# Kernel optimization log

Measured on AMD Instinct MI355X. Metric: run time of the kernel, lower is better.

## Reference

```python
import jax, jax.numpy as jnp
import numpy as np
import math

EMBED_DIM = 1024
N_HEADS = 16
HEAD_DIM = EMBED_DIM // N_HEADS
B, N = 2, 2048


def setup_inputs() -> dict:
    key = jax.random.key(0)
    k1, k2, k3 = jax.random.split(key, 3)
    x = jax.random.normal(k1, (B, N, EMBED_DIM), dtype=jnp.float32)
    # Per-head Linear(D, 3*head_dim), stacked over heads. PyTorch Linear init scale ~1/sqrt(fan_in).
    bound = 1.0 / math.sqrt(EMBED_DIM)
    Wkqv = jax.random.uniform(k2, (N_HEADS, EMBED_DIM, 3 * HEAD_DIM), dtype=jnp.float32, minval=-bound, maxval=bound)
    bkqv = jax.random.uniform(k3, (N_HEADS, 3 * HEAD_DIM), dtype=jnp.float32, minval=-bound, maxval=bound)
    return {"x": x, "Wkqv": Wkqv, "bkqv": bkqv}


def reference(x, Wkqv, bkqv):
    Bx, Nx, D = x.shape
    hd = Wkqv.shape[-1] // 3
    # all heads at once: [B, H, N, 3*hd]
    proj = jnp.einsum('bnd,hdf->bhnf', x, Wkqv) + bkqv[None, :, None, :]
    # torch.split order in the original is (k, q, v)
    k, q, v = jnp.split(proj, 3, axis=-1)
    # scores = q @ k^T / sqrt(head_dim)   [B, H, N, N]
    scores = jnp.einsum('bhqd,bhkd->bhqk', q, k) / math.sqrt(hd)
    causal = jnp.tril(jnp.ones((Nx, Nx), dtype=bool))
    scores = jnp.where(causal[None, None, :, :], scores, -jnp.inf)
    attn = jax.nn.softmax(scores, axis=-1)
    out = jnp.einsum('bhqk,bhkd->bhqd', attn, v)  # [B, H, N, hd]
    # concat heads -> [B, N, D]  (forward() passes no out_matrix, so no output projection)
    return out.transpose(0, 2, 1, 3).reshape(Bx, Nx, D)
```

## Files before the change

### kernel.cpp

```cpp
#include <hip/hip_runtime.h>
#include <math.h>

typedef float f32x4 __attribute__((ext_vector_type(4)));
typedef __bf16 bf16x8 __attribute__((ext_vector_type(8)));
typedef __bf16 bf16x4 __attribute__((ext_vector_type(4)));

#define MFMA16(a, b, c) __builtin_amdgcn_mfma_f32_16x16x32_bf16((a), (b), (c), 0, 0, 0)

constexpr int Bsz = 2, Nseq = 2048, Dm = 1024, Hh = 16, HDim = 64, F3 = 192;
constexpr int Mrows = Bsz * Nseq;
constexpr int NC = Hh * F3;
constexpr float QSCALE = 0.125f * 1.4426950408889634f;

__device__ inline void load_lds16(const void* g, void* l) {
    __builtin_amdgcn_global_load_lds((const __attribute__((address_space(1))) void*)g,
                                     (__attribute__((address_space(3))) void*)l, 16, 0, 0);
}

#define FENCE asm volatile("" ::: "memory")
#define BARRIER do { FENCE; __builtin_amdgcn_s_barrier(); FENCE; } while (0)


__global__ __launch_bounds__(256) void conv_xw_kernel(const float* __restrict__ x,
                                                      __bf16* __restrict__ xb,
                                                      const float* __restrict__ w,
                                                      __bf16* __restrict__ wt) {
    __shared__ __bf16 tile[32][66];
    if (blockIdx.x < 2048) {
        int i = blockIdx.x * 256 + threadIdx.x;
        const float4* xv = reinterpret_cast<const float4*>(x);
        float4 a = xv[2 * i];
        float4 b = xv[2 * i + 1];
        bf16x8 o = {(__bf16)a.x, (__bf16)a.y, (__bf16)a.z, (__bf16)a.w,
                    (__bf16)b.x, (__bf16)b.y, (__bf16)b.z, (__bf16)b.w};
        *reinterpret_cast<bf16x8*>(xb + 8 * i) = o;
    } else {
        int id = blockIdx.x - 2048;
        int h = id / 96, rem = id % 96;
        int d0 = (rem & 31) * 32, c0 = (rem >> 5) * 64;
        for (int i = threadIdx.x; i < 32 * 64; i += 256) {
            int di = i >> 6, cj = i & 63;
            tile[di][cj] = (__bf16)w[(size_t)(h * Dm + d0 + di) * F3 + c0 + cj];
        }
        __syncthreads();
        for (int i = threadIdx.x; i < 32 * 64; i += 256) {
            int ci = i >> 5, dj = i & 31;
            wt[(size_t)(h * F3 + c0 + ci) * Dm + d0 + dj] = tile[dj][ci];
        }
    }
}

__global__ __launch_bounds__(256) void conv_w_kernel(const float* __restrict__ w,
                                                     __bf16* __restrict__ wt) {
    __shared__ __bf16 tile[32][66];
    int h = blockIdx.z, d0 = blockIdx.x * 32, c0 = blockIdx.y * 64;
    for (int i = threadIdx.x; i < 32 * 64; i += 256) {
        int di = i >> 6, cj = i & 63;
        tile[di][cj] = (__bf16)w[(size_t)(h * Dm + d0 + di) * F3 + c0 + cj];
    }
    __syncthreads();
    for (int i = threadIdx.x; i < 32 * 64; i += 256) {
        int ci = i >> 5, dj = i & 31;
        wt[(size_t)(h * F3 + c0 + ci) * Dm + d0 + dj] = tile[dj][ci];
    }
}

__global__ __launch_bounds__(512, 4) void gemm_proj(const __bf16* __restrict__ xb,
                                                    const __bf16* __restrict__ wt,
                                                    const float* __restrict__ bias,
                                                    __bf16* __restrict__ kbuf,
                                                    __bf16* __restrict__ qbuf,
                                                    __bf16* __restrict__ vt) {
    __shared__ __align__(16) __bf16 Ab[2][128 * 64];
    __shared__ __align__(16) __bf16 Bb[2][192 * 64];

    int flat = blockIdx.x;
    int swz = (flat & 7) * 64 + (flat >> 3);
    int bm = swz >> 4, bn = swz & 15;
    int r0 = bm * 128, n0 = bn * 192;

    int w = threadIdx.x >> 6, lane = threadIdx.x & 63;
    int col = lane & 15, quad = lane >> 4;
    int wm = w >> 2, wn = w & 3;

    f32x4 acc[4][3] = {};

    int rl = lane >> 3;
    int cg = ((lane & 7) ^ rl) * 8;

    auto stage = [&](int t, int s) {
#pragma unroll
        for (int i = 0; i < 2; i++) {
            int rowb = w * 16 + i * 8;
            load_lds16(xb + (size_t)(r0 + rowb + rl) * Dm + t * 64 + cg,
                       &Ab[s][rowb * 64]);
        }
#pragma unroll
        for (int i = 0; i < 3; i++) {
            int rowb = w * 24 + i * 8;
            load_lds16(wt + (size_t)(n0 + rowb + rl) * Dm + t * 64 + cg,
                       &Bb[s][rowb * 64]);
        }
    };

    stage(0, 0);
    stage(1, 1);

    for (int j = 0; j < 16; j++) {
        int s = j & 1;
        if (j < 15) asm volatile("s_waitcnt vmcnt(5)" ::: "memory");
        else        asm volatile("s_waitcnt vmcnt(0)" ::: "memory");
        BARRIER;

#pragma unroll
        for (int ks = 0; ks < 2; ks++) {
            int cq = ks * 4 + quad;
            bf16x8 af[4], bfr[3];
#pragma unroll
            for (int mt = 0; mt < 4; mt++) {
                int row = wm * 64 + mt * 16 + col;
                af[mt] = *reinterpret_cast<const bf16x8*>(
                    &Ab[s][row * 64 + ((cq ^ (row & 7)) * 8)]);
            }
#pragma unroll
            for (int nt = 0; nt < 3; nt++) {
                int row = wn * 48 + nt * 16 + col;
                bfr[nt] = *reinterpret_cast<const bf16x8*>(
                    &Bb[s][row * 64 + ((cq ^ (row & 7)) * 8)]);
            }
            __builtin_amdgcn_s_setprio(1);
#pragma unroll
            for (int mt = 0; mt < 4; mt++)
#pragma unroll
                for (int nt = 0; nt < 3; nt++)
                    acc[mt][nt] = MFMA16(af[mt], bfr[nt], acc[mt][nt]);
            __builtin_amdgcn_s_setprio(0);
        }

        BARRIER;
        if (j + 2 < 16) stage(j + 2, s);
    }

#pragma unroll
    for (int nt = 0; nt < 3; nt++) {
        int g = n0 + wn * 48 + nt * 16 + col;
        int h = g / F3, c = g - h * F3;
        float bv = bias[g];
        bool isq = (c >= 64 && c < 128), isv = (c >= 128);
        int cd = c & 63;
#pragma unroll
        for (int mt = 0; mt < 4; mt++) {
#pragma unroll
            for (int rg = 0; rg < 4; rg++) {
                int r = r0 + wm * 64 + mt * 16 + quad * 4 + rg;
                int b = r >> 11, n = r & (Nseq - 1);
                float v = acc[mt][nt][rg] + bv;
                if (isq) v *= QSCALE;
                size_t bh = (size_t)(b * Hh + h);
                if (isv) {
                    int np = (n & ~63) | ((n & 15) << 2) | ((n >> 4) & 3);
                    vt[(bh * HDim + cd) * Nseq + np] = (__bf16)v;
                } else {
                    ((isq) ? qbuf : kbuf)[(bh * Nseq + n) * HDim + cd] = (__bf16)v;
                }
            }
        }
    }
}

__global__ __launch_bounds__(256) void proj_small(const float* __restrict__ x,
                                                  const __bf16* __restrict__ wt,
                                                  const float* __restrict__ bias,
                                                  __bf16* __restrict__ kbuf,
                                                  __bf16* __restrict__ qbuf,
                                                  __bf16* __restrict__ vt) {
    int h = blockIdx.y;
    int wave = threadIdx.x >> 6, lane = threadIdx.x & 63;
    int col = lane & 15, quad = lane >> 4;
    int r0 = blockIdx.x * 128 + wave * 32;

    f32x4 acc[12][2] = {};
    const float* xr0 = x + (size_t)(r0 + col) * Dm + quad * 8;
    const float* xr1 = xr0 + 16 * Dm;
    const __bf16* wbase = wt + (size_t)(h * F3 + col) * Dm + quad * 8;

    for (int k0 = 0; k0 < Dm; k0 += 32) {
        float4 a0lo = *reinterpret_cast<const float4*>(xr0 + k0);
        float4 a0hi = *reinterpret_cast<const float4*>(xr0 + k0 + 4);
        float4 a1lo = *reinterpret_cast<const float4*>(xr1 + k0);
        float4 a1hi = *reinterpret_cast<const float4*>(xr1 + k0 + 4);
        bf16x8 a0 = {(__bf16)a0lo.x, (__bf16)a0lo.y, (__bf16)a0lo.z, (__bf16)a0lo.w,
                     (__bf16)a0hi.x, (__bf16)a0hi.y, (__bf16)a0hi.z, (__bf16)a0hi.w};
        bf16x8 a1 = {(__bf16)a1lo.x, (__bf16)a1lo.y, (__bf16)a1lo.z, (__bf16)a1lo.w,
                     (__bf16)a1hi.x, (__bf16)a1hi.y, (__bf16)a1hi.z, (__bf16)a1hi.w};
#pragma unroll
        for (int ct = 0; ct < 12; ct++) {
            bf16x8 bf = *reinterpret_cast<const bf16x8*>(wbase + ct * 16 * Dm + k0);
            acc[ct][0] = MFMA16(a0, bf, acc[ct][0]);
            acc[ct][1] = MFMA16(a1, bf, acc[ct][1]);
        }
    }
#pragma unroll
    for (int ct = 0; ct < 12; ct++) {
        int c = ct * 16 + col;
        float bv = bias[h * F3 + c];
        int cd = c & 63;
        bool isq = (c >= 64 && c < 128), isv = (c >= 128);
#pragma unroll
        for (int rt = 0; rt < 2; rt++) {
#pragma unroll
            for (int rg = 0; rg < 4; rg++) {
                int r = r0 + rt * 16 + quad * 4 + rg;
                int b = r >> 11, n = r & (Nseq - 1);
                float v = acc[ct][rt][rg] + bv;
                if (isq) v *= QSCALE;
                size_t bh = (size_t)(b * Hh + h);
                if (isv) {
                    int np = (n & ~63) | ((n & 15) << 2) | ((n >> 4) & 3);
                    vt[(bh * HDim + cd) * Nseq + np] = (__bf16)v;
                } else {
                    ((isq) ? qbuf : kbuf)[(bh * Nseq + n) * HDim + cd] = (__bf16)v;
                }
            }
        }
    }
}

__global__ __launch_bounds__(256) void attn_kernel(const __bf16* __restrict__ qbuf,
                                                   const __bf16* __restrict__ kbuf,
                                                   const __bf16* __restrict__ vt,
                                                   float* __restrict__ out) {
    __shared__ __align__(16) __bf16 Kb[2][64 * 64];
    __shared__ __align__(16) __bf16 Vb[2][64 * 64];
    __shared__ __align__(16) __bf16 plds[4][16 * 64];
    int bh = blockIdx.x;
    int b = bh >> 4, h = bh & 15;
    int tile = 31 - blockIdx.y;
    int wave = threadIdx.x >> 6, lane = threadIdx.x & 63;
    int col = lane & 15, quad = lane >> 4;
    int q0 = tile * 64 + wave * 16;

    const __bf16* qbase = qbuf + (size_t)bh * Nseq * HDim;
    const __bf16* kbase = kbuf + (size_t)bh * Nseq * HDim;
    const __bf16* vbase = vt + (size_t)bh * HDim * Nseq;

    bf16x8 aq0 = *reinterpret_cast<const bf16x8*>(qbase + (q0 + col) * HDim + quad * 8);
    bf16x8 aq1 = *reinterpret_cast<const bf16x8*>(qbase + (q0 + col) * HDim + quad * 8 + 32);

    const bf16x8 vone = {(__bf16)1.f, (__bf16)1.f, (__bf16)1.f, (__bf16)1.f,
                         (__bf16)1.f, (__bf16)1.f, (__bf16)1.f, (__bf16)1.f};

    f32x4 o[4] = {};
    f32x4 ls = {};

    int mb = tile * 64;
    int loop_end = mb + 64;

    int rl = lane >> 3;
    int srow0 = wave * 16 + rl;
    int srow1 = wave * 16 + 8 + rl;
    int sc = (lane & 7) ^ rl;
    const __bf16* ksrc0 = kbase + srow0 * HDim + sc * 8;
    const __bf16* ksrc1 = kbase + srow1 * HDim + sc * 8;
    const __bf16* vsrc0 = vbase + (size_t)srow0 * Nseq + sc * 8;
    const __bf16* vsrc1 = vbase + (size_t)srow1 * Nseq + sc * 8;
    int d0 = wave * 1024, d1 = wave * 1024 + 512;

    int sw0 = ((quad ^ (col & 7)) * 8);
    int sw1 = (((quad + 4) ^ (col & 7)) * 8);

    int pr0 = col * 64 + ((quad ^ (col & 7)) << 3);
    int pr1 = col * 64 + (((quad + 4) ^ (col & 7)) << 3);

    load_lds16(ksrc0, &Kb[0][d0]);
    load_lds16(ksrc1, &Kb[0][d1]);
    load_lds16(vsrc0, &Vb[0][d0]);
    load_lds16(vsrc1, &Vb[0][d1]);
    FENCE;

    int s = 0;
    for (int kb = 0; kb < loop_end; kb += 64) {
        asm volatile("s_waitcnt vmcnt(0)" ::: "memory");
        BARRIER;
        int nkb = kb + 64;
        load_lds16(ksrc0 + nkb * HDim, &Kb[s ^ 1][d0]);
        load_lds16(ksrc1 + nkb * HDim, &Kb[s ^ 1][d1]);
        load_lds16(vsrc0 + nkb, &Vb[s ^ 1][d0]);
        load_lds16(vsrc1 + nkb, &Vb[s ^ 1][d1]);

        bool masked = (kb == mb);
        const __bf16* Kcur = Kb[s];
        const __bf16* Vcur = Vb[s];
        f32x4 z = {};
        f32x4 sc4[4];
#pragma unroll
        for (int g = 0; g < 4; g++) {
            const __bf16* krow = Kcur + (col + 16 * g) * 64;
            bf16x8 k0 = *reinterpret_cast<const bf16x8*>(krow + sw0);
            bf16x8 k1 = *reinterpret_cast<const bf16x8*>(krow + sw1);
            sc4[g] = MFMA16(aq0, k0, z);
            sc4[g] = MFMA16(aq1, k1, sc4[g]);
        }
        if (masked) {
#pragma unroll
            for (int r = 0; r < 4; r++) {
                int row = quad * 4 + r;
                int qi = q0 + row;
                bf16x4 pk;
#pragma unroll
                for (int g = 0; g < 4; g++) {
                    float p = (kb + col + 16 * g <= qi) ? exp2f(sc4[g][r]) : 0.f;
                    pk[g] = (__bf16)p;
                }
                *reinterpret_cast<bf16x4*>(
                    &plds[wave][row * 64 + ((col ^ ((row & 7) << 1)) << 2)]) = pk;
            }
        } else {
#pragma unroll
            for (int r = 0; r < 4; r++) {
                int row = quad * 4 + r;
                bf16x4 pk;
#pragma unroll
                for (int g = 0; g < 4; g++) pk[g] = (__bf16)exp2f(sc4[g][r]);
                *reinterpret_cast<bf16x4*>(
                    &plds[wave][row * 64 + ((col ^ ((row & 7) << 1)) << 2)]) = pk;
            }
        }
        bf16x8 pa0 = *reinterpret_cast<const bf16x8*>(&plds[wave][pr0]);
        bf16x8 pa1 = *reinterpret_cast<const bf16x8*>(&plds[wave][pr1]);
        ls = MFMA16(pa0, vone, ls);
        ls = MFMA16(pa1, vone, ls);
#pragma unroll
        for (int nt = 0; nt < 4; nt++) {
            const __bf16* vrow = Vcur + (col + 16 * nt) * 64;
            bf16x8 v0 = *reinterpret_cast<const bf16x8*>(vrow + sw0);
            bf16x8 v1 = *reinterpret_cast<const bf16x8*>(vrow + sw1);
            o[nt] = MFMA16(pa0, v0, o[nt]);
            o[nt] = MFMA16(pa1, v1, o[nt]);
        }
        s ^= 1;
    }

    float linv[4];
#pragma unroll
    for (int r = 0; r < 4; r++) linv[r] = 1.f / ls[r];
#pragma unroll
    for (int nt = 0; nt < 4; nt++) {
#pragma unroll
        for (int r = 0; r < 4; r++) {
            int qi = q0 + quad * 4 + r;
            out[((size_t)(b * Nseq + qi)) * Dm + h * HDim + nt * 16 + col] = o[nt][r] * linv[r];
        }
    }
}

extern "C" void kernel_launch(void* const* d_in, const int* in_sizes, int n_in,
                              void* d_out, int out_size, void* d_ws, size_t ws_size,
                              hipStream_t stream) {
    const float* x = nullptr;
    const float* w = nullptr;
    const float* bias = nullptr;
    for (int i = 0; i < n_in; i++) {
        if (in_sizes[i] == Mrows * Dm) x = (const float*)d_in[i];
        else if (in_sizes[i] == Hh * Dm * F3) w = (const float*)d_in[i];
        else if (in_sizes[i] == Hh * F3) bias = (const float*)d_in[i];
    }
    float* outp = (float*)d_out;

    char* ws = (char*)d_ws;
    __bf16* wt = (__bf16*)(ws);
    __bf16* kbuf = (__bf16*)(ws + 6291456);
    __bf16* qbuf = (__bf16*)(ws + 6291456 + 8388608);
    __bf16* vt = (__bf16*)(ws + 6291456 + 2 * 8388608);
    __bf16* xb = (__bf16*)(ws + 6291456 + 3 * 8388608);

    if (ws_size >= (size_t)(6291456 + 4 * 8388608)) {
        conv_xw_kernel<<<3584, 256, 0, stream>>>(x, xb, w, wt);
        gemm_proj<<<dim3((Mrows / 128) * (NC / 192)), 512, 0, stream>>>(xb, wt, bias, kbuf, qbuf, vt);
    } else {
        conv_w_kernel<<<dim3(Dm / 32, F3 / 64, Hh), 256, 0, stream>>>(w, wt);
        proj_small<<<dim3(Mrows / 128, Hh), 256, 0, stream>>>(x, wt, bias, kbuf, qbuf, vt);
    }
    attn_kernel<<<dim3(32, 32), 256, 0, stream>>>(qbuf, kbuf, vt, outp);
}
```

Baseline: 152.9 us.

## Compute transposed scores so P stays in registers, drop LDS round-trip

```diff
diff --git a/kernel.cpp b/kernel.cpp
--- a/kernel.cpp
+++ b/kernel.cpp
@@ -158,7 +158,8 @@
                 if (isq) v *= QSCALE;
                 size_t bh = (size_t)(b * Hh + h);
                 if (isv) {
-                    int np = (n & ~63) | ((n & 15) << 2) | ((n >> 4) & 3);
+                    int np = (n & ~63) | (((n >> 5) & 1) << 5) | ((n & 12) << 1)
+                           | (((n >> 4) & 1) << 2) | (n & 3);
                     vt[(bh * HDim + cd) * Nseq + np] = (__bf16)v;
                 } else {
                     ((isq) ? qbuf : kbuf)[(bh * Nseq + n) * HDim + cd] = (__bf16)v;
@@ -216,7 +217,8 @@
                 if (isq) v *= QSCALE;
                 size_t bh = (size_t)(b * Hh + h);
                 if (isv) {
-                    int np = (n & ~63) | ((n & 15) << 2) | ((n >> 4) & 3);
+                    int np = (n & ~63) | (((n >> 5) & 1) << 5) | ((n & 12) << 1)
+                           | (((n >> 4) & 1) << 2) | (n & 3);
                     vt[(bh * HDim + cd) * Nseq + np] = (__bf16)v;
                 } else {
                     ((isq) ? qbuf : kbuf)[(bh * Nseq + n) * HDim + cd] = (__bf16)v;
@@ -232,7 +234,6 @@
                                                    float* __restrict__ out) {
     __shared__ __align__(16) __bf16 Kb[2][64 * 64];
     __shared__ __align__(16) __bf16 Vb[2][64 * 64];
-    __shared__ __align__(16) __bf16 plds[4][16 * 64];
     int bh = blockIdx.x;
     int b = bh >> 4, h = bh & 15;
     int tile = 31 - blockIdx.y;
@@ -255,6 +256,7 @@
 
     int mb = tile * 64;
     int loop_end = mb + 64;
+    int qi = q0 + col;
 
     int rl = lane >> 3;
     int srow0 = wave * 16 + rl;
@@ -269,9 +271,6 @@
     int sw0 = ((quad ^ (col & 7)) * 8);
     int sw1 = (((quad + 4) ^ (col & 7)) * 8);
 
-    int pr0 = col * 64 + ((quad ^ (col & 7)) << 3);
-    int pr1 = col * 64 + (((quad + 4) ^ (col & 7)) << 3);
-
     load_lds16(ksrc0, &Kb[0][d0]);
     load_lds16(ksrc1, &Kb[0][d1]);
     load_lds16(vsrc0, &Vb[0][d0]);
@@ -298,36 +297,30 @@
             const __bf16* krow = Kcur + (col + 16 * g) * 64;
             bf16x8 k0 = *reinterpret_cast<const bf16x8*>(krow + sw0);
             bf16x8 k1 = *reinterpret_cast<const bf16x8*>(krow + sw1);
-            sc4[g] = MFMA16(aq0, k0, z);
-            sc4[g] = MFMA16(aq1, k1, sc4[g]);
-        }
+            sc4[g] = MFMA16(k0, aq0, z);
+            sc4[g] = MFMA16(k1, aq1, sc4[g]);
+        }
+        bf16x8 pa0, pa1;
         if (masked) {
 #pragma unroll
-            for (int r = 0; r < 4; r++) {
-                int row = quad * 4 + r;
-                int qi = q0 + row;
-                bf16x4 pk;
-#pragma unroll
-                for (int g = 0; g < 4; g++) {
-                    float p = (kb + col + 16 * g <= qi) ? exp2f(sc4[g][r]) : 0.f;
-                    pk[g] = (__bf16)p;
+            for (int g = 0; g < 4; g++)
+#pragma unroll
+                for (int r = 0; r < 4; r++) {
+                    int key = kb + 16 * g + quad * 4 + r;
+                    float p = (key <= qi) ? exp2f(sc4[g][r]) : 0.f;
+                    if (g < 2) pa0[(g & 1) * 4 + r] = (__bf16)p;
+                    else       pa1[(g & 1) * 4 + r] = (__bf16)p;
                 }
-                *reinterpret_cast<bf16x4*>(
-                    &plds[wave][row * 64 + ((col ^ ((row & 7) << 1)) << 2)]) = pk;
-            }
         } else {
 #pragma unroll
-            for (int r = 0; r < 4; r++) {
-                int row = quad * 4 + r;
-                bf16x4 pk;
-#pragma unroll
-                for (int g = 0; g < 4; g++) pk[g] = (__bf16)exp2f(sc4[g][r]);
-                *reinterpret_cast<bf16x4*>(
-                    &plds[wave][row * 64 + ((col ^ ((row & 7) << 1)) << 2)]) = pk;
-            }
-        }
-        bf16x8 pa0 = *reinterpret_cast<const bf16x8*>(&plds[wave][pr0]);
-        bf16x8 pa1 = *reinterpret_cast<const bf16x8*>(&plds[wave][pr1]);
+            for (int g = 0; g < 4; g++)
+#pragma unroll
+                for (int r = 0; r < 4; r++) {
+                    float p = exp2f(sc4[g][r]);
+                    if (g < 2) pa0[(g & 1) * 4 + r] = (__bf16)p;
+                    else       pa1[(g & 1) * 4 + r] = (__bf16)p;
+                }
+        }
         ls = MFMA16(pa0, vone, ls);
         ls = MFMA16(pa1, vone, ls);
 #pragma unroll
@@ -348,8 +341,8 @@
     for (int nt = 0; nt < 4; nt++) {
 #pragma unroll
         for (int r = 0; r < 4; r++) {
-            int qi = q0 + quad * 4 + r;
-            out[((size_t)(b * Nseq + qi)) * Dm + h * HDim + nt * 16 + col] = o[nt][r] * linv[r];
+            int qr = q0 + quad * 4 + r;
+            out[((size_t)(b * Nseq + qr)) * Dm + h * HDim + nt * 16 + col] = o[nt][r] * linv[r];
         }
     }
 }
```

Result: faster. 145.3 us (-5.0%).
